# Kernel optimization log

Measured on AMD Instinct MI355X. Metric: run time of the kernel, lower is better.

## Reference

```python
import jax, jax.numpy as jnp
import numpy as np

TEMPERATURE = 8.0  # sqrt(d_head=64)


def setup_inputs() -> dict:
    key = jax.random.key(0)
    ks = jax.random.split(key, 6)
    shape = (4, 16, 2048, 64)  # [B, H, L, d_head]
    names = ["q_real", "q_imag", "k_real", "k_imag", "v_real", "v_imag"]
    return {n: jax.random.normal(k, shape, dtype=jnp.float32) for n, k in zip(names, ks)}


def reference(q_real, q_imag, k_real, k_imag, v_real, v_imag):
    # attn = | (q / T) @ conj(k)^H |
    # complex matmul with b = conj(k)^T: br = k_r^T, bi = -k_i^T
    qr = q_real / TEMPERATURE
    qi = q_imag / TEMPERATURE
    # [B,H,Lq,Lk]
    s_real = jnp.einsum("bhqd,bhkd->bhqk", qr, k_real) + jnp.einsum("bhqd,bhkd->bhqk", qi, k_imag)
    s_imag = jnp.einsum("bhqd,bhkd->bhqk", qi, k_real) - jnp.einsum("bhqd,bhkd->bhqk", qr, k_imag)
    attn = jax.nn.softmax(jnp.sqrt(s_real * s_real + s_imag * s_imag), axis=-1)
    # dropout p=0.0 (eval) -> identity
    out_real = jnp.einsum("bhqk,bhkd->bhqd", attn, v_real)
    out_imag = jnp.einsum("bhqk,bhkd->bhqd", attn, v_imag)
    # torch.view_as_complex(stack([real, imag], -1)) -> represent as stacked last dim
    output = jnp.stack([out_real, out_imag], axis=-1)  # [B,H,L,d,2]
    return output, attn
```

## Files before the change

kernel.cpp:

```cpp
#include <hip/hip_runtime.h>
#include <hip/hip_bf16.h>

constexpr int kL  = 2048;
constexpr int kD  = 64;
constexpr int kBH = 64;
constexpr size_t kAttnOff = (size_t)kBH * kL * kD * 2;

typedef __bf16 bf16x8 __attribute__((ext_vector_type(8)));
typedef __bf16 bf16x4 __attribute__((ext_vector_type(4)));
typedef float  f32x4  __attribute__((ext_vector_type(4)));
typedef unsigned int u32x4 __attribute__((ext_vector_type(4)));

static __device__ inline bf16x8 neg8(bf16x8 v) {
  u32x4 t = __builtin_bit_cast(u32x4, v);
  t ^= 0x80008000u;
  return __builtin_bit_cast(bf16x8, t);
}

static __device__ inline bf16x8 pack8(const float4& a, const float4& b) {
  bf16x8 p;
  p[0]=(__bf16)a.x; p[1]=(__bf16)a.y; p[2]=(__bf16)a.z; p[3]=(__bf16)a.w;
  p[4]=(__bf16)b.x; p[5]=(__bf16)b.y; p[6]=(__bf16)b.z; p[7]=(__bf16)b.w;
  return p;
}

static __device__ inline void gl_lds16(char* l, const char* g) {
  __builtin_amdgcn_global_load_lds(
      (const __attribute__((address_space(1))) void*)g,
      (__attribute__((address_space(3))) void*)l, 16, 0, 0);
}

__global__ __launch_bounds__(256) void prep_k_kernel(
    const float* __restrict__ kr_g, const float* __restrict__ ki_g,
    __hip_bfloat16* __restrict__ kb_r, __hip_bfloat16* __restrict__ kb_i)
{
  const int tid = threadIdx.x;
  const int bh  = blockIdx.x >> 5;
  const int kb  = blockIdx.x & 31;
  const int k0  = kb * 64;
  const size_t tb = ((size_t)bh * 32 + kb) * 8192;

  const int row = tid >> 2;
  const int d0  = (tid & 3) << 4;
  const size_t gb = ((size_t)bh * kL + k0 + row) * kD + d0;
  const int swz = (row & 7) << 4;

  float4 x0 = *(const float4*)(kr_g + gb);
  float4 x1 = *(const float4*)(kr_g + gb + 4);
  float4 x2 = *(const float4*)(kr_g + gb + 8);
  float4 x3 = *(const float4*)(kr_g + gb + 12);
  *(bf16x8*)((char*)kb_r + tb + row * 128 + ((d0 * 2) ^ swz))      = pack8(x0, x1);
  *(bf16x8*)((char*)kb_r + tb + row * 128 + ((d0 * 2 + 16) ^ swz)) = pack8(x2, x3);
  float4 y0 = *(const float4*)(ki_g + gb);
  float4 y1 = *(const float4*)(ki_g + gb + 4);
  float4 y2 = *(const float4*)(ki_g + gb + 8);
  float4 y3 = *(const float4*)(ki_g + gb + 12);
  *(bf16x8*)((char*)kb_i + tb + row * 128 + ((d0 * 2) ^ swz))      = pack8(y0, y1);
  *(bf16x8*)((char*)kb_i + tb + row * 128 + ((d0 * 2 + 16) ^ swz)) = pack8(y2, y3);
}

__global__ __launch_bounds__(256) void prep_v_kernel(
    const float* __restrict__ vr_g, const float* __restrict__ vi_g,
    __hip_bfloat16* __restrict__ vt_r, __hip_bfloat16* __restrict__ vt_i)
{
  __shared__ __align__(16) char lds_raw[2 * 8192];
  char* tr = lds_raw;
  char* ti = lds_raw + 8192;

  const int tid = threadIdx.x;
  const int bh  = blockIdx.x >> 5;
  const int kb  = blockIdx.x & 31;
  const int k0  = kb * 64;
  const size_t tb = ((size_t)bh * 32 + kb) * 8192;

  {
    const int row = tid >> 2;
    const int d0  = (tid & 3) << 4;
    const size_t gb = ((size_t)bh * kL + k0 + row) * kD + d0;
    const int swz = (row & 7) << 4;
    float4 x0 = *(const float4*)(vr_g + gb);
    float4 x1 = *(const float4*)(vr_g + gb + 4);
    float4 x2 = *(const float4*)(vr_g + gb + 8);
    float4 x3 = *(const float4*)(vr_g + gb + 12);
    *(bf16x8*)(tr + row * 128 + ((d0 * 2) ^ swz))      = pack8(x0, x1);
    *(bf16x8*)(tr + row * 128 + ((d0 * 2 + 16) ^ swz)) = pack8(x2, x3);
    float4 y0 = *(const float4*)(vi_g + gb);
    float4 y1 = *(const float4*)(vi_g + gb + 4);
    float4 y2 = *(const float4*)(vi_g + gb + 8);
    float4 y3 = *(const float4*)(vi_g + gb + 12);
    *(bf16x8*)(ti + row * 128 + ((d0 * 2) ^ swz))      = pack8(y0, y1);
    *(bf16x8*)(ti + row * 128 + ((d0 * 2 + 16) ^ swz)) = pack8(y2, y3);
  }
  __syncthreads();
  {
    const int d  = tid >> 2;
    const int kc = (tid & 3) << 4;
    char* outr = (char*)vt_r + tb + d * 128;
    char* outi = (char*)vt_i + tb + d * 128;
    const int oswz = (d & 7) << 4;
    bf16x8 pr0, pr1, pi0, pi1;
#pragma unroll
    for (int j = 0; j < 8; ++j) {
      const int k1 = kc + j;
      const int k2 = kc + 8 + j;
      const int b1 = k1 * 128 + ((d * 2) ^ ((k1 & 7) << 4));
      const int b2 = k2 * 128 + ((d * 2) ^ ((k2 & 7) << 4));
      pr0[j] = *(const __bf16*)(tr + b1);
      pr1[j] = *(const __bf16*)(tr + b2);
      pi0[j] = *(const __bf16*)(ti + b1);
      pi1[j] = *(const __bf16*)(ti + b2);
    }
    *(bf16x8*)(outr + ((kc * 2) ^ oswz))      = pr0;
    *(bf16x8*)(outr + ((kc * 2 + 16) ^ oswz)) = pr1;
    *(bf16x8*)(outi + ((kc * 2) ^ oswz))      = pi0;
    *(bf16x8*)(outi + ((kc * 2 + 16) ^ oswz)) = pi1;
  }
}

__global__ __launch_bounds__(256) void qk_ews(
    const float* __restrict__ qr_g, const float* __restrict__ qi_g,
    const __hip_bfloat16* __restrict__ kb_r, const __hip_bfloat16* __restrict__ kb_i,
    __hip_bfloat16* __restrict__ ews, float* __restrict__ rowsum)
{
  __shared__ __align__(16) char lds_raw[49152];
  char* e_l = lds_raw + 32768 + (threadIdx.x >> 6) * 4096;

  const int tid  = threadIdx.x;
  const int wave = tid >> 6;
  const int lane = tid & 63;
  const int g    = lane >> 4;
  const int r    = lane & 15;

  const int bid = blockIdx.x;
  const int nid = (bid & 7) * 128 + (bid >> 3);
  const int bh  = nid >> 4;
  const int q0w = (nid & 15) * 128 + wave * 32;

  bf16x8 aqr[2][2], aqi[2][2], aqrn[2][2];
#pragma unroll
  for (int qt = 0; qt < 2; ++qt) {
    const size_t qbase = ((size_t)bh * kL + q0w + qt * 16 + r) * kD + g * 8;
#pragma unroll
    for (int f = 0; f < 2; ++f) {
      float4 x0 = *(const float4*)(qr_g + qbase + f * 32);
      float4 x1 = *(const float4*)(qr_g + qbase + f * 32 + 4);
      float4 y0 = *(const float4*)(qi_g + qbase + f * 32);
      float4 y1 = *(const float4*)(qi_g + qbase + f * 32 + 4);
      float xr[8] = {x0.x, x0.y, x0.z, x0.w, x1.x, x1.y, x1.z, x1.w};
      float xi[8] = {y0.x, y0.y, y0.z, y0.w, y1.x, y1.y, y1.z, y1.w};
#pragma unroll
      for (int i = 0; i < 8; ++i) {
        aqr[qt][f][i] = (__bf16)(xr[i] * 0.125f);
        aqi[qt][f][i] = (__bf16)(xi[i] * 0.125f);
      }
      aqrn[qt][f] = neg8(aqr[qt][f]);
    }
  }

  float rs[2] = {0.f, 0.f};
  const int off1 = tid * 16;
  const int off2 = off1 + 4096;
  const size_t tbase = (size_t)bh * 32 * 8192;

  auto ISSUE = [&](char* buf, int t) {
    const char* sr = (const char*)kb_r + tbase + (size_t)t * 8192;
    const char* si = (const char*)kb_i + tbase + (size_t)t * 8192;
    gl_lds16(buf + off1, sr + off1);
    gl_lds16(buf + off2, sr + off2);
    gl_lds16(buf + 8192 + off1, si + off1);
    gl_lds16(buf + 8192 + off2, si + off2);
  };

  ISSUE(lds_raw, 0);

#pragma unroll 1
  for (int t = 0; t < 32; ++t) {
    char* cbuf = lds_raw + (t & 1) * 16384;
    char* nbuf = lds_raw + ((t + 1) & 1) * 16384;
    if (t == 0) asm volatile("s_waitcnt vmcnt(0)" ::: "memory");
    else        asm volatile("s_waitcnt vmcnt(4)" ::: "memory");
    __builtin_amdgcn_s_barrier();
    __builtin_amdgcn_sched_barrier(0);
    if (t < 31) ISSUE(nbuf, t + 1);
    const int k0 = t * 64;

#pragma unroll
    for (int s = 0; s < 4; ++s) {
      const int krow = s * 16 + r;
      const int swz  = (krow & 7) << 4;
      bf16x8 bkr[2], bki[2];
#pragma unroll
      for (int f = 0; f < 2; ++f) {
        const int byte = krow * 128 + (((f * 32 + g * 8) * 2) ^ swz);
        bkr[f] = *(const bf16x8*)(cbuf + byte);
        bki[f] = *(const bf16x8*)(cbuf + 8192 + byte);
      }
#pragma unroll
      for (int qt = 0; qt < 2; ++qt) {
        f32x4 accr = {0.f, 0.f, 0.f, 0.f};
        f32x4 acci = {0.f, 0.f, 0.f, 0.f};
#pragma unroll
        for (int f = 0; f < 2; ++f) {
          accr = __builtin_amdgcn_mfma_f32_16x16x32_bf16(bkr[f], aqr[qt][f],  accr, 0, 0, 0);
          accr = __builtin_amdgcn_mfma_f32_16x16x32_bf16(bki[f], aqi[qt][f],  accr, 0, 0, 0);
          acci = __builtin_amdgcn_mfma_f32_16x16x32_bf16(bkr[f], aqi[qt][f],  acci, 0, 0, 0);
          acci = __builtin_amdgcn_mfma_f32_16x16x32_bf16(bki[f], aqrn[qt][f], acci, 0, 0, 0);
        }
        float e[4];
#pragma unroll
        for (int i = 0; i < 4; ++i)
          e[i] = __expf(sqrtf(accr[i] * accr[i] + acci[i] * acci[i]));
        rs[qt] += (e[0] + e[1]) + (e[2] + e[3]);
        bf16x4 pe;
#pragma unroll
        for (int i = 0; i < 4; ++i) pe[i] = (__bf16)e[i];
        const int row = qt * 16 + r;
        *(bf16x4*)(e_l + row * 128 + (((s * 16 + g * 4) * 2) ^ ((row & 7) << 4))) = pe;
      }
    }

#pragma unroll
    for (int m = 0; m < 4; ++m) {
      const int row  = m * 8 + (lane >> 3);
      const int byte = row * 128 + (((lane & 7) * 16) ^ ((row & 7) << 4));
      bf16x8 v = *(const bf16x8*)(e_l + byte);
      const size_t base = ((size_t)bh * kL + q0w + row) * kL + k0 + (lane & 7) * 8;
      *(bf16x8*)((__bf16*)ews + base) = v;
    }
  }

#pragma unroll
  for (int qt = 0; qt < 2; ++qt) {
    rs[qt] += __shfl_xor(rs[qt], 16, 64);
    rs[qt] += __shfl_xor(rs[qt], 32, 64);
  }
  if (lane < 16) {
#pragma unroll
    for (int qt = 0; qt < 2; ++qt)
      rowsum[(size_t)bh * kL + q0w + qt * 16 + lane] = rs[qt];
  }
}

__global__ __launch_bounds__(256) void pv_norm(
    const __hip_bfloat16* __restrict__ vt_r, const __hip_bfloat16* __restrict__ vt_i,
    const __hip_bfloat16* __restrict__ ews, float* __restrict__ attn,
    const float* __restrict__ rowsum, float* __restrict__ out)
{
  __shared__ __align__(16) char lds_raw[32768];

  const int tid  = threadIdx.x;
  const int wave = tid >> 6;
  const int lane = tid & 63;
  const int g    = lane >> 4;
  const int r    = lane & 15;

  const int bid = blockIdx.x;
  const int nid = (bid & 7) * 128 + (bid >> 3);
  const int bh  = nid >> 4;
  const int q0w = (nid & 15) * 128 + wave * 32;

  float invA[2];
  size_t ebase[2];
#pragma unroll
  for (int qt = 0; qt < 2; ++qt) {
    invA[qt]  = 1.0f / rowsum[(size_t)bh * kL + q0w + qt * 16 + r];
    ebase[qt] = ((size_t)bh * kL + q0w + qt * 16 + r) * kL;
  }

  f32x4 o_r[2][4], o_i[2][4];
#pragma unroll
  for (int qt = 0; qt < 2; ++qt)
#pragma unroll
    for (int dt = 0; dt < 4; ++dt) {
      o_r[qt][dt] = (f32x4){0.f, 0.f, 0.f, 0.f};
      o_i[qt][dt] = (f32x4){0.f, 0.f, 0.f, 0.f};
    }

  const int off1 = tid * 16;
  const int off2 = off1 + 4096;
  const size_t tbase = (size_t)bh * 32 * 8192;

  auto ISSUE = [&](char* buf, int t) {
    const char* sr = (const char*)vt_r + tbase + (size_t)t * 8192;
    const char* si = (const char*)vt_i + tbase + (size_t)t * 8192;
    gl_lds16(buf + off1, sr + off1);
    gl_lds16(buf + off2, sr + off2);
    gl_lds16(buf + 8192 + off1, si + off1);
    gl_lds16(buf + 8192 + off2, si + off2);
  };

  ISSUE(lds_raw, 0);

#pragma unroll 1
  for (int t = 0; t < 32; ++t) {
    char* cbuf = lds_raw + (t & 1) * 16384;
    char* nbuf = lds_raw + ((t + 1) & 1) * 16384;
    if (t == 0) asm volatile("s_waitcnt vmcnt(0)" ::: "memory");
    else        asm volatile("s_waitcnt vmcnt(8)" ::: "memory");
    __builtin_amdgcn_s_barrier();
    __builtin_amdgcn_sched_barrier(0);
    if (t < 31) ISSUE(nbuf, t + 1);
    const int k0 = t * 64;

    bf16x8 ef[2][2];
#pragma unroll
    for (int kh = 0; kh < 2; ++kh)
#pragma unroll
      for (int qt = 0; qt < 2; ++qt) {
        const size_t eb = ebase[qt] + k0 + kh * 32 + g * 8;
        bf16x8 v = *(const bf16x8*)((const __bf16*)ews + eb);
        ef[kh][qt] = v;
        float4 w0, w1;
        w0.x = (float)v[0] * invA[qt]; w0.y = (float)v[1] * invA[qt];
        w0.z = (float)v[2] * invA[qt]; w0.w = (float)v[3] * invA[qt];
        w1.x = (float)v[4] * invA[qt]; w1.y = (float)v[5] * invA[qt];
        w1.z = (float)v[6] * invA[qt]; w1.w = (float)v[7] * invA[qt];
        *(float4*)(attn + eb)     = w0;
        *(float4*)(attn + eb + 4) = w1;
      }

#pragma unroll
    for (int kh = 0; kh < 2; ++kh)
#pragma unroll
      for (int dt = 0; dt < 4; ++dt) {
        const int d = dt * 16 + r;
        const int byte = d * 128 + (((kh * 32 + g * 8) * 2) ^ ((d & 7) << 4));
        bf16x8 bvr = *(const bf16x8*)(cbuf + byte);
        bf16x8 bvi = *(const bf16x8*)(cbuf + 8192 + byte);
#pragma unroll
        for (int qt = 0; qt < 2; ++qt) {
          o_r[qt][dt] = __builtin_amdgcn_mfma_f32_16x16x32_bf16(ef[kh][qt], bvr, o_r[qt][dt], 0, 0, 0);
          o_i[qt][dt] = __builtin_amdgcn_mfma_f32_16x16x32_bf16(ef[kh][qt], bvi, o_i[qt][dt], 0, 0, 0);
        }
      }
  }

#pragma unroll
  for (int qt = 0; qt < 2; ++qt)
#pragma unroll
    for (int i = 0; i < 4; ++i) {
      const size_t q = q0w + qt * 16 + g * 4 + i;
      const float iv = 1.0f / rowsum[(size_t)bh * kL + q];
#pragma unroll
      for (int dt = 0; dt < 4; ++dt) {
        const int d = dt * 16 + r;
        float2 val;
        val.x = o_r[qt][dt][i] * iv;
        val.y = o_i[qt][dt][i] * iv;
        *(float2*)(out + (((size_t)bh * kL + q) * kD + d) * 2) = val;
      }
    }
}

__global__ __launch_bounds__(256) void qk_exp_legacy(
    const float* __restrict__ qr_g, const float* __restrict__ qi_g,
    const float* __restrict__ kr_g, const float* __restrict__ ki_g,
    float* __restrict__ attn, float* __restrict__ rowsum)
{
  __shared__ __align__(16) char lds_raw[16384 + 4 * 4096];
  char* kr_l = lds_raw;
  char* ki_l = lds_raw + 8192;
  char* e_l  = lds_raw + 16384 + (threadIdx.x >> 6) * 4096;

  const int tid  = threadIdx.x;
  const int wave = tid >> 6;
  const int lane = tid & 63;
  const int g    = lane >> 4;
  const int r    = lane & 15;

  const int bid = blockIdx.x;
  const int nid = (bid & 7) * 128 + (bid >> 3);
  const int bh  = nid >> 4;
  const int q0w = (nid & 15) * 128 + wave * 32;

  bf16x8 aqr[2][2], aqi[2][2];
#pragma unroll
  for (int qt = 0; qt < 2; ++qt) {
    const size_t qbase = ((size_t)bh * kL + q0w + qt * 16 + r) * kD + g * 8;
#pragma unroll
    for (int f = 0; f < 2; ++f) {
      float4 x0 = *(const float4*)(qr_g + qbase + f * 32);
      float4 x1 = *(const float4*)(qr_g + qbase + f * 32 + 4);
      float4 y0 = *(const float4*)(qi_g + qbase + f * 32);
      float4 y1 = *(const float4*)(qi_g + qbase + f * 32 + 4);
      float xr[8] = {x0.x, x0.y, x0.z, x0.w, x1.x, x1.y, x1.z, x1.w};
      float xi[8] = {y0.x, y0.y, y0.z, y0.w, y1.x, y1.y, y1.z, y1.w};
#pragma unroll
      for (int i = 0; i < 8; ++i) {
        aqr[qt][f][i] = (__bf16)(xr[i] * 0.125f);
        aqi[qt][f][i] = (__bf16)(xi[i] * 0.125f);
      }
    }
  }

  float rs[2] = {0.f, 0.f};

  for (int k0 = 0; k0 < kL; k0 += 64) {
    __syncthreads();
    {
      const int row = tid >> 2;
      const int d0  = (tid & 3) << 4;
      const size_t gb = ((size_t)bh * kL + k0 + row) * kD + d0;
      const int base = row * 128;
      const int swz  = (row & 7) << 4;
      {
        float4 x0 = *(const float4*)(kr_g + gb);
        float4 x1 = *(const float4*)(kr_g + gb + 4);
        float4 x2 = *(const float4*)(kr_g + gb + 8);
        float4 x3 = *(const float4*)(kr_g + gb + 12);
        *(bf16x8*)(kr_l + base + ((d0 * 2) ^ swz))      = pack8(x0, x1);
        *(bf16x8*)(kr_l + base + ((d0 * 2 + 16) ^ swz)) = pack8(x2, x3);
      }
      {
        float4 x0 = *(const float4*)(ki_g + gb);
        float4 x1 = *(const float4*)(ki_g + gb + 4);
        float4 x2 = *(const float4*)(ki_g + gb + 8);
        float4 x3 = *(const float4*)(ki_g + gb + 12);
        *(bf16x8*)(ki_l + base + ((d0 * 2) ^ swz))      = pack8(x0, x1);
        *(bf16x8*)(ki_l + base + ((d0 * 2 + 16) ^ swz)) = pack8(x2, x3);
      }
    }
    __syncthreads();

#pragma unroll
    for (int s = 0; s < 4; ++s) {
      const int krow = s * 16 + r;
      const int swz  = (krow & 7) << 4;
      bf16x8 bkr[2], bki[2], bkin[2];
#pragma unroll
      for (int f = 0; f < 2; ++f) {
        const int byte = krow * 128 + (((f * 32 + g * 8) * 2) ^ swz);
        bkr[f]  = *(const bf16x8*)(kr_l + byte);
        bki[f]  = *(const bf16x8*)(ki_l + byte);
        bkin[f] = neg8(bki[f]);
      }
#pragma unroll
      for (int qt = 0; qt < 2; ++qt) {
        f32x4 accr = {0.f, 0.f, 0.f, 0.f};
        f32x4 acci = {0.f, 0.f, 0.f, 0.f};
#pragma unroll
        for (int f = 0; f < 2; ++f) {
          accr = __builtin_amdgcn_mfma_f32_16x16x32_bf16(bkr[f],  aqr[qt][f], accr, 0, 0, 0);
          accr = __builtin_amdgcn_mfma_f32_16x16x32_bf16(bki[f],  aqi[qt][f], accr, 0, 0, 0);
          acci = __builtin_amdgcn_mfma_f32_16x16x32_bf16(bkr[f],  aqi[qt][f], acci, 0, 0, 0);
          acci = __builtin_amdgcn_mfma_f32_16x16x32_bf16(bkin[f], aqr[qt][f], acci, 0, 0, 0);
        }
        float e[4];
#pragma unroll
        for (int i = 0; i < 4; ++i)
          e[i] = __expf(sqrtf(accr[i] * accr[i] + acci[i] * acci[i]));
        rs[qt] += (e[0] + e[1]) + (e[2] + e[3]);
        bf16x4 pe;
#pragma unroll
        for (int i = 0; i < 4; ++i) pe[i] = (__bf16)e[i];
        const int row = qt * 16 + r;
        *(bf16x4*)(e_l + row * 128 + (((s * 16 + g * 4) * 2) ^ ((row & 7) << 4))) = pe;
      }
    }

#pragma unroll
    for (int m = 0; m < 4; ++m) {
      const int row  = m * 8 + (lane >> 3);
      const int byte = row * 128 + (((lane & 7) * 16) ^ ((row & 7) << 4));
      bf16x8 v = *(const bf16x8*)(e_l + byte);
      const size_t base = ((size_t)bh * kL + q0w + row) * kL + k0 + (lane & 7) * 8;
      float4 w0, w1;
      w0.x=(float)v[0]; w0.y=(float)v[1]; w0.z=(float)v[2]; w0.w=(float)v[3];
      w1.x=(float)v[4]; w1.y=(float)v[5]; w1.z=(float)v[6]; w1.w=(float)v[7];
      *(float4*)(attn + base)     = w0;
      *(float4*)(attn + base + 4) = w1;
    }
  }

#pragma unroll
  for (int qt = 0; qt < 2; ++qt) {
    rs[qt] += __shfl_xor(rs[qt], 16, 64);
    rs[qt] += __shfl_xor(rs[qt], 32, 64);
  }
  if (lane < 16) {
#pragma unroll
    for (int qt = 0; qt < 2; ++qt)
      rowsum[(size_t)bh * kL + q0w + qt * 16 + lane] = rs[qt];
  }
}

__global__ __launch_bounds__(256) void pv_legacy(
    const float* __restrict__ vr_g, const float* __restrict__ vi_g,
    float* __restrict__ attn, const float* __restrict__ rowsum,
    float* __restrict__ out)
{
  __shared__ __align__(16) char lds_raw[2 * 8192];
  char* vr_l = lds_raw;
  char* vi_l = lds_raw + 8192;

  const int tid  = threadIdx.x;
  const int wave = tid >> 6;
  const int lane = tid & 63;
  const int g    = lane >> 4;
  const int r    = lane & 15;

  const int bid = blockIdx.x;
  const int nid = (bid & 7) * 128 + (bid >> 3);
  const int bh  = nid >> 4;
  const int q0w = (nid & 15) * 128 + wave * 32;

  float invA[2];
#pragma unroll
  for (int qt = 0; qt < 2; ++qt)
    invA[qt] = 1.0f / rowsum[(size_t)bh * kL + q0w + qt * 16 + r];

  f32x4 o_r[2][4], o_i[2][4];
#pragma unroll
  for (int qt = 0; qt < 2; ++qt)
#pragma unroll
    for (int dt = 0; dt < 4; ++dt) {
      o_r[qt][dt] = (f32x4){0.f, 0.f, 0.f, 0.f};
      o_i[qt][dt] = (f32x4){0.f, 0.f, 0.f, 0.f};
    }

  for (int k0 = 0; k0 < kL; k0 += 64) {
    __syncthreads();
    {
      const int p  = tid >> 3;
      const int d0 = (tid & 7) << 3;
      const size_t gb0 = ((size_t)bh * kL + k0 + 2 * p) * kD + d0;
      const size_t gb1 = gb0 + kD;
      float4 a0 = *(const float4*)(vr_g + gb0);
      float4 a1 = *(const float4*)(vr_g + gb0 + 4);
      float4 a2 = *(const float4*)(vr_g + gb1);
      float4 a3 = *(const float4*)(vr_g + gb1 + 4);
      float4 b0 = *(const float4*)(vi_g + gb0);
      float4 b1 = *(const float4*)(vi_g + gb0 + 4);
      float4 b2 = *(const float4*)(vi_g + gb1);
      float4 b3 = *(const float4*)(vi_g + gb1 + 4);
      float vr0[8] = {a0.x, a0.y, a0.z, a0.w, a1.x, a1.y, a1.z, a1.w};
      float vr1[8] = {a2.x, a2.y, a2.z, a2.w, a3.x, a3.y, a3.z, a3.w};
      float vi0[8] = {b0.x, b0.y, b0.z, b0.w, b1.x, b1.y, b1.z, b1.w};
      float vi1[8] = {b2.x, b2.y, b2.z, b2.w, b3.x, b3.y, b3.z, b3.w};
#pragma unroll
      for (int j = 0; j < 8; ++j) {
        const int d = d0 + j;
        const int byte = d * 128 + ((p * 4) ^ ((d & 7) << 4));
        __bf16 pa[2] = {(__bf16)vr0[j], (__bf16)vr1[j]};
        __bf16 pb[2] = {(__bf16)vi0[j], (__bf16)vi1[j]};
        *(unsigned int*)(vr_l + byte) = *(unsigned int*)pa;
        *(unsigned int*)(vi_l + byte) = *(unsigned int*)pb;
      }
    }
    __syncthreads();

#pragma unroll
    for (int kh = 0; kh < 2; ++kh) {
      bf16x8 af[2];
#pragma unroll
      for (int qt = 0; qt < 2; ++qt) {
        const size_t q = q0w + qt * 16 + r;
        const size_t eb = ((size_t)bh * kL + q) * kL + k0 + kh * 32 + g * 8;
        float4 e0 = *(const float4*)(attn + eb);
        float4 e1 = *(const float4*)(attn + eb + 4);
        af[qt][0]=(__bf16)e0.x; af[qt][1]=(__bf16)e0.y; af[qt][2]=(__bf16)e0.z; af[qt][3]=(__bf16)e0.w;
        af[qt][4]=(__bf16)e1.x; af[qt][5]=(__bf16)e1.y; af[qt][6]=(__bf16)e1.z; af[qt][7]=(__bf16)e1.w;
        float4 w0 = {e0.x * invA[qt], e0.y * invA[qt], e0.z * invA[qt], e0.w * invA[qt]};
        float4 w1 = {e1.x * invA[qt], e1.y * invA[qt], e1.z * invA[qt], e1.w * invA[qt]};
        *(float4*)(attn + eb)     = w0;
        *(float4*)(attn + eb + 4) = w1;
      }
#pragma unroll
      for (int dt = 0; dt < 4; ++dt) {
        const int d = dt * 16 + r;
        const int byte = d * 128 + (((kh * 32 + g * 8) * 2) ^ ((d & 7) << 4));
        bf16x8 bvr = *(const bf16x8*)(vr_l + byte);
        bf16x8 bvi = *(const bf16x8*)(vi_l + byte);
#pragma unroll
        for (int qt = 0; qt < 2; ++qt) {
          o_r[qt][dt] = __builtin_amdgcn_mfma_f32_16x16x32_bf16(af[qt], bvr, o_r[qt][dt], 0, 0, 0);
          o_i[qt][dt] = __builtin_amdgcn_mfma_f32_16x16x32_bf16(af[qt], bvi, o_i[qt][dt], 0, 0, 0);
        }
      }
    }
  }

#pragma unroll
  for (int qt = 0; qt < 2; ++qt)
#pragma unroll
    for (int i = 0; i < 4; ++i) {
      const size_t q = q0w + qt * 16 + g * 4 + i;
      const float iv = 1.0f / rowsum[(size_t)bh * kL + q];
#pragma unroll
      for (int dt = 0; dt < 4; ++dt) {
        const int d = dt * 16 + r;
        float2 val;
        val.x = o_r[qt][dt][i] * iv;
        val.y = o_i[qt][dt][i] * iv;
        *(float2*)(out + (((size_t)bh * kL + q) * kD + d) * 2) = val;
      }
    }
}

extern "C" void kernel_launch(void* const* d_in, const int* in_sizes, int n_in,
                              void* d_out, int out_size, void* d_ws, size_t ws_size,
                              hipStream_t stream) {
  const float* qr = (const float*)d_in[0];
  const float* qi = (const float*)d_in[1];
  const float* kr = (const float*)d_in[2];
  const float* ki = (const float*)d_in[3];
  const float* vr = (const float*)d_in[4];
  const float* vi = (const float*)d_in[5];
  float* out  = (float*)d_out;
  float* attn = out + kAttnOff;

  const size_t rowsum_bytes = (size_t)kBH * kL * 4;
  const size_t e_bytes      = (size_t)kBH * kL * kL * 2;
  const size_t tile_bytes   = (size_t)kBH * kL * kD * 2;
  float* rowsum = (float*)d_ws;
  __hip_bfloat16* ews = (__hip_bfloat16*)((char*)d_ws + rowsum_bytes);
  char* tiles = (char*)d_ws + rowsum_bytes + e_bytes;
  __hip_bfloat16* t0 = (__hip_bfloat16*)(tiles);
  __hip_bfloat16* t1 = (__hip_bfloat16*)(tiles + tile_bytes);

  dim3 gridP(kBH * (kL / 64));
  dim3 gridM(kBH * (kL / 128));

  if (ws_size >= rowsum_bytes + e_bytes + 2 * tile_bytes) {
    prep_k_kernel<<<gridP, 256, 0, stream>>>(kr, ki, t0, t1);
    qk_ews<<<gridM, 256, 0, stream>>>(qr, qi, t0, t1, ews, rowsum);
    prep_v_kernel<<<gridP, 256, 0, stream>>>(vr, vi, t0, t1);
    pv_norm<<<gridM, 256, 0, stream>>>(t0, t1, ews, attn, rowsum, out);
  } else {
    qk_exp_legacy<<<gridM, 256, 0, stream>>>(qr, qi, kr, ki, attn, rowsum);
    pv_legacy<<<gridM, 256, 0, stream>>>(vr, vi, attn, rowsum, out);
  }
}
```

Measured before the change: 679.7 us.

## Merge K/V prep kernels and software-pipeline exp-score loads in PV kernel

Replaces the separate K and V preparation launches with one kernel that converts K and transposes V into separate workspace buffers, removing a launch and letting qk_ews and pv_norm run back to back. In pv_norm the loop is unrolled by two with explicit double buffers, so each step's bf16 exp-score loads from global memory are issued one chunk ahead and overlap the MFMA work. An extra sched_barrier is added in qk_ews to keep the tile issue ahead of compute. This needs twice the tile workspace, and the hand-set vmcnt counts must match the new outstanding-load pattern.

```diff
diff --git a/kernel.cpp b/kernel.cpp
--- a/kernel.cpp
+++ b/kernel.cpp
@@ -28,6 +28,82 @@
   __builtin_amdgcn_global_load_lds(
       (const __attribute__((address_space(1))) void*)g,
       (__attribute__((address_space(3))) void*)l, 16, 0, 0);
+}
+
+__global__ __launch_bounds__(256) void prep_all_kernel(
+    const float* __restrict__ kr_g, const float* __restrict__ ki_g,
+    const float* __restrict__ vr_g, const float* __restrict__ vi_g,
+    __hip_bfloat16* __restrict__ kb_r, __hip_bfloat16* __restrict__ kb_i,
+    __hip_bfloat16* __restrict__ vt_r, __hip_bfloat16* __restrict__ vt_i)
+{
+  __shared__ __align__(16) char lds_raw[2 * 8192];
+  char* tr = lds_raw;
+  char* ti = lds_raw + 8192;
+
+  const int tid = threadIdx.x;
+  const int bh  = blockIdx.x >> 5;
+  const int kb  = blockIdx.x & 31;
+  const int k0  = kb * 64;
+  const size_t tb = ((size_t)bh * 32 + kb) * 8192;
+
+  const int row = tid >> 2;
+  const int d0  = (tid & 3) << 4;
+  const size_t gb = ((size_t)bh * kL + k0 + row) * kD + d0;
+  const int swz = (row & 7) << 4;
+
+  {
+    float4 x0 = *(const float4*)(kr_g + gb);
+    float4 x1 = *(const float4*)(kr_g + gb + 4);
+    float4 x2 = *(const float4*)(kr_g + gb + 8);
+    float4 x3 = *(const float4*)(kr_g + gb + 12);
+    *(bf16x8*)((char*)kb_r + tb + row * 128 + ((d0 * 2) ^ swz))      = pack8(x0, x1);
+    *(bf16x8*)((char*)kb_r + tb + row * 128 + ((d0 * 2 + 16) ^ swz)) = pack8(x2, x3);
+    float4 y0 = *(const float4*)(ki_g + gb);
+    float4 y1 = *(const float4*)(ki_g + gb + 4);
+    float4 y2 = *(const float4*)(ki_g + gb + 8);
+    float4 y3 = *(const float4*)(ki_g + gb + 12);
+    *(bf16x8*)((char*)kb_i + tb + row * 128 + ((d0 * 2) ^ swz))      = pack8(y0, y1);
+    *(bf16x8*)((char*)kb_i + tb + row * 128 + ((d0 * 2 + 16) ^ swz)) = pack8(y2, y3);
+  }
+
+  {
+    float4 x0 = *(const float4*)(vr_g + gb);
+    float4 x1 = *(const float4*)(vr_g + gb + 4);
+    float4 x2 = *(const float4*)(vr_g + gb + 8);
+    float4 x3 = *(const float4*)(vr_g + gb + 12);
+    *(bf16x8*)(tr + row * 128 + ((d0 * 2) ^ swz))      = pack8(x0, x1);
+    *(bf16x8*)(tr + row * 128 + ((d0 * 2 + 16) ^ swz)) = pack8(x2, x3);
+    float4 y0 = *(const float4*)(vi_g + gb);
+    float4 y1 = *(const float4*)(vi_g + gb + 4);
+    float4 y2 = *(const float4*)(vi_g + gb + 8);
+    float4 y3 = *(const float4*)(vi_g + gb + 12);
+    *(bf16x8*)(ti + row * 128 + ((d0 * 2) ^ swz))      = pack8(y0, y1);
+    *(bf16x8*)(ti + row * 128 + ((d0 * 2 + 16) ^ swz)) = pack8(y2, y3);
+  }
+  __syncthreads();
+  {
+    const int d  = tid >> 2;
+    const int kc = (tid & 3) << 4;
+    char* outr = (char*)vt_r + tb + d * 128;
+    char* outi = (char*)vt_i + tb + d * 128;
+    const int oswz = (d & 7) << 4;
+    bf16x8 pr0, pr1, pi0, pi1;
+#pragma unroll
+    for (int j = 0; j < 8; ++j) {
+      const int k1 = kc + j;
+      const int k2 = kc + 8 + j;
+      const int b1 = k1 * 128 + ((d * 2) ^ ((k1 & 7) << 4));
+      const int b2 = k2 * 128 + ((d * 2) ^ ((k2 & 7) << 4));
+      pr0[j] = *(const __bf16*)(tr + b1);
+      pr1[j] = *(const __bf16*)(tr + b2);
+      pi0[j] = *(const __bf16*)(ti + b1);
+      pi1[j] = *(const __bf16*)(ti + b2);
+    }
+    *(bf16x8*)(outr + ((kc * 2) ^ oswz))      = pr0;
+    *(bf16x8*)(outr + ((kc * 2 + 16) ^ oswz)) = pr1;
+    *(bf16x8*)(outi + ((kc * 2) ^ oswz))      = pi0;
+    *(bf16x8*)(outi + ((kc * 2 + 16) ^ oswz)) = pi1;
+  }
 }
 
 __global__ __launch_bounds__(256) void prep_k_kernel(
@@ -182,6 +258,7 @@
     __builtin_amdgcn_s_barrier();
     __builtin_amdgcn_sched_barrier(0);
     if (t < 31) ISSUE(nbuf, t + 1);
+    __builtin_amdgcn_sched_barrier(0);
     const int k0 = t * 64;
 
 #pragma unroll
@@ -279,6 +356,8 @@
   const int off1 = tid * 16;
   const int off2 = off1 + 4096;
   const size_t tbase = (size_t)bh * 32 * 8192;
+  char* buf0 = lds_raw;
+  char* buf1 = lds_raw + 16384;
 
   auto ISSUE = [&](char* buf, int t) {
     const char* sr = (const char*)vt_r + tbase + (size_t)t * 8192;
@@ -289,27 +368,23 @@
     gl_lds16(buf + 8192 + off2, si + off2);
   };
 
-  ISSUE(lds_raw, 0);
-
-#pragma unroll 1
-  for (int t = 0; t < 32; ++t) {
-    char* cbuf = lds_raw + (t & 1) * 16384;
-    char* nbuf = lds_raw + ((t + 1) & 1) * 16384;
-    if (t == 0) asm volatile("s_waitcnt vmcnt(0)" ::: "memory");
-    else        asm volatile("s_waitcnt vmcnt(8)" ::: "memory");
-    __builtin_amdgcn_s_barrier();
-    __builtin_amdgcn_sched_barrier(0);
-    if (t < 31) ISSUE(nbuf, t + 1);
+  bf16x8 efA[2][2], efB[2][2];
+  auto LOADE = [&](int t, bf16x8 (&ef)[2][2]) {
+#pragma unroll
+    for (int kh = 0; kh < 2; ++kh)
+#pragma unroll
+      for (int qt = 0; qt < 2; ++qt)
+        ef[kh][qt] = *(const bf16x8*)((const __bf16*)ews + ebase[qt] + t * 64 + kh * 32 + g * 8);
+  };
+
+  auto CHUNK = [&](int t, bf16x8 (&ef)[2][2], const char* cbuf) {
     const int k0 = t * 64;
-
-    bf16x8 ef[2][2];
 #pragma unroll
     for (int kh = 0; kh < 2; ++kh)
 #pragma unroll
       for (int qt = 0; qt < 2; ++qt) {
         const size_t eb = ebase[qt] + k0 + kh * 32 + g * 8;
-        bf16x8 v = *(const bf16x8*)((const __bf16*)ews + eb);
-        ef[kh][qt] = v;
+        bf16x8 v = ef[kh][qt];
         float4 w0, w1;
         w0.x = (float)v[0] * invA[qt]; w0.y = (float)v[1] * invA[qt];
         w0.z = (float)v[2] * invA[qt]; w0.w = (float)v[3] * invA[qt];
@@ -318,7 +393,6 @@
         *(float4*)(attn + eb)     = w0;
         *(float4*)(attn + eb + 4) = w1;
       }
-
 #pragma unroll
     for (int kh = 0; kh < 2; ++kh)
 #pragma unroll
@@ -333,6 +407,34 @@
           o_i[qt][dt] = __builtin_amdgcn_mfma_f32_16x16x32_bf16(ef[kh][qt], bvi, o_i[qt][dt], 0, 0, 0);
         }
       }
+  };
+
+  ISSUE(buf0, 0);
+  __builtin_amdgcn_sched_barrier(0);
+  LOADE(0, efA);
+
+#pragma unroll 1
+  for (int t = 0; t < 32; t += 2) {
+    if (t == 0) asm volatile("s_waitcnt vmcnt(4)" ::: "memory");
+    else        asm volatile("s_waitcnt vmcnt(12)" ::: "memory");
+    __builtin_amdgcn_s_barrier();
+    __builtin_amdgcn_sched_barrier(0);
+    ISSUE(buf1, t + 1);
+    __builtin_amdgcn_sched_barrier(0);
+    LOADE(t + 1, efB);
+    __builtin_amdgcn_sched_barrier(0);
+    CHUNK(t, efA, buf0);
+
+    asm volatile("s_waitcnt vmcnt(12)" ::: "memory");
+    __builtin_amdgcn_s_barrier();
+    __builtin_amdgcn_sched_barrier(0);
+    if (t + 2 < 32) {
+      ISSUE(buf0, t + 2);
+      __builtin_amdgcn_sched_barrier(0);
+      LOADE(t + 2, efA);
+      __builtin_amdgcn_sched_barrier(0);
+    }
+    CHUNK(t + 1, efB, buf1);
   }
 
 #pragma unroll
@@ -617,11 +719,17 @@
   char* tiles = (char*)d_ws + rowsum_bytes + e_bytes;
   __hip_bfloat16* t0 = (__hip_bfloat16*)(tiles);
   __hip_bfloat16* t1 = (__hip_bfloat16*)(tiles + tile_bytes);
+  __hip_bfloat16* t2 = (__hip_bfloat16*)(tiles + 2 * tile_bytes);
+  __hip_bfloat16* t3 = (__hip_bfloat16*)(tiles + 3 * tile_bytes);
 
   dim3 gridP(kBH * (kL / 64));
   dim3 gridM(kBH * (kL / 128));
 
-  if (ws_size >= rowsum_bytes + e_bytes + 2 * tile_bytes) {
+  if (ws_size >= rowsum_bytes + e_bytes + 4 * tile_bytes) {
+    prep_all_kernel<<<gridP, 256, 0, stream>>>(kr, ki, vr, vi, t0, t1, t2, t3);
+    qk_ews<<<gridM, 256, 0, stream>>>(qr, qi, t0, t1, ews, rowsum);
+    pv_norm<<<gridM, 256, 0, stream>>>(t2, t3, ews, attn, rowsum, out);
+  } else if (ws_size >= rowsum_bytes + e_bytes + 2 * tile_bytes) {
     prep_k_kernel<<<gridP, 256, 0, stream>>>(kr, ki, t0, t1);
     qk_ews<<<gridM, 256, 0, stream>>>(qr, qi, t0, t1, ews, rowsum);
     prep_v_kernel<<<gridP, 256, 0, stream>>>(vr, vi, t0, t1);
```

After: 687.5 us. Within noise of the previous version (+1.1%).
